# Kernel optimization log

Measured on AMD Instinct MI355X. Metric: run time of the kernel, lower is better.

## Reference

```python
import jax, jax.numpy as jnp
import numpy as np

N_A, N_B = 50000, 50000
E = 500000
IN, H, OUT, NGRAPHS = 128, 128, 10, 64
# (src_type, dst_type) per edge type, matching metadata[1]
EDGE_TYPES = [(0, 0), (0, 1), (1, 0), (1, 1)]
NUM_LAYERS = 2
NEG_SLOPE = 0.2  # GATConv leaky_relu slope


def setup_inputs() -> dict:
    key = jax.random.key(0)
    ks = jax.random.split(key, 16)
    ei = [jax.random.randint(ks[2 + e], (2, E), 0, 50000).astype(jnp.int32) for e in range(4)]
    return {
        "x_A": jax.random.normal(ks[0], (N_A, IN), jnp.float32),
        "x_B": jax.random.normal(ks[1], (N_B, IN), jnp.float32),
        "ei0": ei[0], "ei1": ei[1], "ei2": ei[2], "ei3": ei[3],
        "batch_A": jnp.sort(jax.random.randint(ks[6], (N_A,), 0, NGRAPHS)).astype(jnp.int32),
        "batch_B": jnp.sort(jax.random.randint(ks[7], (N_B,), 0, NGRAPHS)).astype(jnp.int32),
        "batch_size": NGRAPHS,
        "w_src": jax.random.normal(ks[8], (NUM_LAYERS, 4, IN, H), jnp.float32) * 0.05,
        "w_dst": jax.random.normal(ks[9], (NUM_LAYERS, 4, IN, H), jnp.float32) * 0.05,
        "att_src": jax.random.normal(ks[10], (NUM_LAYERS, 4, H), jnp.float32) * 0.05,
        "att_dst": jax.random.normal(ks[11], (NUM_LAYERS, 4, H), jnp.float32) * 0.05,
        "conv_bias": jax.random.normal(ks[12], (NUM_LAYERS, 4, H), jnp.float32) * 0.05,
        "wc": jax.random.normal(ks[13], (2 * H, OUT), jnp.float32) * 0.05,
        "bc": jax.random.normal(ks[14], (OUT,), jnp.float32) * 0.05,
    }


def gat_conv(x_src, x_dst, edge_index, ws, wd, a_s, a_d, b, num_dst):
    # PyG GATConv, heads=1, add_self_loops=False, aggr='mean'
    h_src = x_src @ ws            # [Ns, H]
    h_dst = x_dst @ wd            # [Nd, H]
    s_src = h_src @ a_s           # [Ns]
    s_dst = h_dst @ a_d           # [Nd]
    src, dst = edge_index[0], edge_index[1]
    score = jax.nn.leaky_relu(s_src[src] + s_dst[dst], NEG_SLOPE)  # [E]
    # segment softmax over destination nodes
    smax = jax.ops.segment_max(score, dst, num_segments=num_dst)
    ex = jnp.exp(score - smax[dst])
    denom = jax.ops.segment_sum(ex, dst, num_segments=num_dst)
    alpha = ex / denom[dst]
    msg = alpha[:, None] * h_src[src]                               # [E, H]
    summed = jax.ops.segment_sum(msg, dst, num_segments=num_dst)
    cnt = jax.ops.segment_sum(jnp.ones_like(alpha), dst, num_segments=num_dst)
    return summed / jnp.maximum(cnt, 1.0)[:, None] + b


def mean_pool(x, batch, batch_size):
    s = jax.ops.segment_sum(x, batch, num_segments=batch_size)
    c = jax.ops.segment_sum(jnp.ones((x.shape[0],), x.dtype), batch, num_segments=batch_size)
    return s / jnp.maximum(c, 1.0)[:, None]


def reference(x_A, x_B, ei0, ei1, ei2, ei3, batch_A, batch_B, batch_size,
              w_src, w_dst, att_src, att_dst, conv_bias, wc, bc):
    xs = [x_A, x_B]
    eis = [ei0, ei1, ei2, ei3]
    for L in range(NUM_LAYERS):
        outs = {0: [], 1: []}
        for e, (st, dt) in enumerate(EDGE_TYPES):
            o = gat_conv(xs[st], xs[dt], eis[e], w_src[L, e], w_dst[L, e],
                         att_src[L, e], att_dst[L, e], conv_bias[L, e], xs[dt].shape[0])
            outs[dt].append(o)
        # HeteroConv inter_aggr='mean' across edge types, then relu (dropout is identity in eval)
        xs = [jax.nn.relu(jnp.mean(jnp.stack(outs[t], 0), 0)) for t in (0, 1)]
    pooled = [mean_pool(xs[0], batch_A, batch_size), mean_pool(xs[1], batch_B, batch_size)]
    graph_emb = jnp.concatenate(pooled, axis=1)  # [B, 2H]
    return graph_emb @ wc + bc
```

## Files before the change

kernel.cpp:

```cpp
#include <hip/hip_runtime.h>
#include <hip/hip_bf16.h>

#define NN 50000
#define EE 500000
#define GG 64
#define NSL 50
#define SPAN 1000
#define NCH 125
#define EPG (EE / NCH)
#define NCNT (4 * NSL * NCH)
#define SCB ((NCNT + 255) / 256)

typedef __attribute__((ext_vector_type(8))) short bf16x8;
typedef __attribute__((ext_vector_type(4))) float f32x4;

__device__ __forceinline__ float wred_sum(float v) {
#pragma unroll
  for (int s = 32; s; s >>= 1) v += __shfl_xor(v, s, 64);
  return v;
}
__device__ __forceinline__ float gred_sum(float v) {
  v += __shfl_xor(v, 1, 64);
  v += __shfl_xor(v, 2, 64);
  v += __shfl_xor(v, 4, 64);
  v += __shfl_xor(v, 8, 64);
  return v;
}
__device__ __forceinline__ float gred_max(float v) {
  v = fmaxf(v, __shfl_xor(v, 1, 64));
  v = fmaxf(v, __shfl_xor(v, 2, 64));
  v = fmaxf(v, __shfl_xor(v, 4, 64));
  v = fmaxf(v, __shfl_xor(v, 8, 64));
  return v;
}

__device__ __forceinline__ short f2bf(float x) {
  __hip_bfloat16 b = __float2bfloat16(x);
  return *reinterpret_cast<short*>(&b);
}
__device__ __forceinline__ float bf2f(unsigned short s) {
  __hip_bfloat16 b = *reinterpret_cast<__hip_bfloat16*>(&s);
  return __bfloat162float(b);
}

__global__ __launch_bounds__(256) void v_kernel(const float* wdst, const float* adst, float* v) {
  int wv = (blockIdx.x * 256 + threadIdx.x) >> 6;
  int lane = threadIdx.x & 63;
  int le = wv >> 7, k = wv & 127;
  const float* W = wdst + (size_t)le * 16384 + k * 128;
  const float* a = adst + le * 128;
  float p = W[lane] * a[lane] + W[64 + lane] * a[64 + lane];
  p = wred_sum(p);
  if (lane == 0) v[le * 128 + k] = p;
}

__global__ __launch_bounds__(256) void wcvt_kernel(const float* wsrc, short* whiT, short* wloT) {
  int idx = blockIdx.x * 256 + threadIdx.x;
  int le = idx >> 14, rem = idx & 16383;
  int c = rem >> 7, k = rem & 127;
  float v = wsrc[(size_t)le * 16384 + k * 128 + c];
  short hi = f2bf(v);
  whiT[idx] = hi;
  wloT[idx] = f2bf(v - bf2f((unsigned short)hi));
}


__global__ __launch_bounds__(256) void pcount_kernel(const int* e0, const int* e1, const int* e2,
                                                     const int* e3, int* counts) {
  int t = blockIdx.y, ch = blockIdx.x;
  const int* ei = (t == 0 ? e0 : t == 1 ? e1 : t == 2 ? e2 : e3);
  const int* dst = ei + EE;
  __shared__ int cnt[NSL];
  for (int i = threadIdx.x; i < NSL; i += 256) cnt[i] = 0;
  __syncthreads();
  int i0 = ch * EPG;
  for (int i = i0 + threadIdx.x; i < i0 + EPG; i += 256) atomicAdd(&cnt[dst[i] / SPAN], 1);
  __syncthreads();
  for (int sl = threadIdx.x; sl < NSL; sl += 256) counts[(t * NSL + sl) * NCH + ch] = cnt[sl];
}

__global__ __launch_bounds__(256) void scan1_kernel(const int* counts, int* bsums) {
  int tid = threadIdx.x, lane = tid & 63, wid = tid >> 6;
  int idx = blockIdx.x * 256 + tid;
  int v = (idx < NCNT) ? counts[idx] : 0;
#pragma unroll
  for (int s = 32; s; s >>= 1) v += __shfl_xor(v, s, 64);
  __shared__ int ws[4];
  if (lane == 0) ws[wid] = v;
  __syncthreads();
  if (tid == 0) bsums[blockIdx.x] = ws[0] + ws[1] + ws[2] + ws[3];
}

__global__ void scan2_kernel(int* bsums) {
  __shared__ int s[SCB];
  int tid = threadIdx.x;
  if (tid < SCB) s[tid] = bsums[tid];
  __syncthreads();
  if (tid == 0) {
    int run = 0;
    for (int i = 0; i < SCB; i++) { int x = s[i]; s[i] = run; run += x; }
  }
  __syncthreads();
  if (tid < SCB) bsums[tid] = s[tid];
}

__global__ __launch_bounds__(256) void scan3_kernel(int* counts, const int* bsums, int* sliceptr) {
  int tid = threadIdx.x, lane = tid & 63, wid = tid >> 6;
  int idx = blockIdx.x * 256 + tid;
  int v = (idx < NCNT) ? counts[idx] : 0;
  int orig = v;
#pragma unroll
  for (int s = 1; s < 64; s <<= 1) { int u = __shfl_up(v, s, 64); if (lane >= s) v += u; }
  __shared__ int ws[4];
  if (lane == 63) ws[wid] = v;
  __syncthreads();
  int woff = (wid > 0 ? ws[0] : 0) + (wid > 1 ? ws[1] : 0) + (wid > 2 ? ws[2] : 0);
  int excl = bsums[blockIdx.x] + woff + v - orig;
  if (idx < NCNT) {
    counts[idx] = excl;
    if (idx % NCH == 0) {
      int g = idx / NCH;
      sliceptr[(g / NSL) * (NSL + 1) + (g % NSL)] = excl;
    }
  }
  if (blockIdx.x == 0 && tid < 4) sliceptr[tid * (NSL + 1) + NSL] = (tid + 1) * EE;
}

__global__ __launch_bounds__(256) void ppart_kernel(const int* e0, const int* e1, const int* e2,
                                                    const int* e3, const int* counts, int2* pairs) {
  int t = blockIdx.y, ch = blockIdx.x;
  const int* ei = (t == 0 ? e0 : t == 1 ? e1 : t == 2 ? e2 : e3);
  const int* srcr = ei;
  const int* dstr = ei + EE;
  __shared__ int cur[NSL];
  for (int i = threadIdx.x; i < NSL; i += 256) cur[i] = counts[(t * NSL + i) * NCH + ch];
  __syncthreads();
  int i0 = ch * EPG;
  for (int i = i0 + threadIdx.x; i < i0 + EPG; i += 256) {
    int d = dstr[i], s = srcr[i];
    int pos = atomicAdd(&cur[d / SPAN], 1);
    pairs[pos] = make_int2(s, d);
  }
}

__global__ __launch_bounds__(256) void pbuild_kernel(const int2* pairs, const int* sliceptr,
                                                     int* rowptr, int* col) {
  int t = blockIdx.y, sl = blockIdx.x;
  int n0 = sl * SPAN;
  int e0 = sliceptr[t * (NSL + 1) + sl], e1 = sliceptr[t * (NSL + 1) + sl + 1];
  int tid = threadIdx.x, lane = tid & 63, wid = tid >> 6;
  __shared__ int cnt[SPAN];
  __shared__ int wsum[4];
  for (int i = tid; i < SPAN; i += 256) cnt[i] = 0;
  __syncthreads();
  for (int e = e0 + tid; e < e1; e += 256) atomicAdd(&cnt[pairs[e].y - n0], 1);
  __syncthreads();
  int s0 = 0, s1 = 0, s2 = 0, s3 = 0, tot = 0;
  if (tid < SPAN / 4) {
    s0 = cnt[tid * 4]; s1 = cnt[tid * 4 + 1]; s2 = cnt[tid * 4 + 2]; s3 = cnt[tid * 4 + 3];
    tot = s0 + s1 + s2 + s3;
  }
  int v = tot;
#pragma unroll
  for (int sft = 1; sft < 64; sft <<= 1) { int u = __shfl_up(v, sft, 64); if (lane >= sft) v += u; }
  if (lane == 63) wsum[wid] = v;
  __syncthreads();
  int woffv = (wid > 0 ? wsum[0] : 0) + (wid > 1 ? wsum[1] : 0) + (wid > 2 ? wsum[2] : 0);
  int excl = v + woffv - tot;
  __syncthreads();
  if (tid < SPAN / 4) {
    cnt[tid * 4] = excl;
    cnt[tid * 4 + 1] = excl + s0;
    cnt[tid * 4 + 2] = excl + s0 + s1;
    cnt[tid * 4 + 3] = excl + s0 + s1 + s2;
  }
  __syncthreads();
  int base = e0 - t * EE;
  for (int n = tid; n < SPAN; n += 256) rowptr[(size_t)t * (NN + 1) + n0 + n] = base + cnt[n];
  if (sl == NSL - 1 && tid == 0) rowptr[(size_t)t * (NN + 1) + NN] = EE;
  __syncthreads();
  int* ct = col + (size_t)t * EE;
  for (int e = e0 + tid; e < e1; e += 256) {
    int2 p = pairs[e];
    int pos = base + atomicAdd(&cnt[p.y - n0], 1);
    ct[pos] = p.x;
  }
}

__global__ void gbound_kernel(const int* batchA, const int* batchB, int* gbA, int* gbB) {
  int t = threadIdx.x;
  if (t >= 130) return;
  int which = t / 65, g = t % 65;
  const int* b = which ? batchB : batchA;
  int* gb = which ? gbB : gbA;
  int lo = 0, hi = NN;
  while (lo < hi) { int mid = (lo + hi) >> 1; if (b[mid] < g) lo = mid + 1; else hi = mid; }
  gb[g] = lo;
}

#define SWZ(row, kb) ((((row) << 6) + (kb)) ^ (((row) & 7) << 4))
#define HSTRIDE 132

__device__ __forceinline__ void cvt8(const float4 a, const float4 b, bf16x8& hv, bf16x8& lv) {
  short h;
  h = f2bf(a.x); hv[0] = h; lv[0] = f2bf(a.x - bf2f((unsigned short)h));
  h = f2bf(a.y); hv[1] = h; lv[1] = f2bf(a.y - bf2f((unsigned short)h));
  h = f2bf(a.z); hv[2] = h; lv[2] = f2bf(a.z - bf2f((unsigned short)h));
  h = f2bf(a.w); hv[3] = h; lv[3] = f2bf(a.w - bf2f((unsigned short)h));
  h = f2bf(b.x); hv[4] = h; lv[4] = f2bf(b.x - bf2f((unsigned short)h));
  h = f2bf(b.y); hv[5] = h; lv[5] = f2bf(b.y - bf2f((unsigned short)h));
  h = f2bf(b.z); hv[6] = h; lv[6] = f2bf(b.z - bf2f((unsigned short)h));
  h = f2bf(b.w); hv[7] = h; lv[7] = f2bf(b.w - bf2f((unsigned short)h));
}

__global__ __launch_bounds__(256) void gemm_hs_kernel(
    const float* XA, const short* WhA, const short* WlA, const float* attA, unsigned short* hAo, float* sAo,
    const float* XB, const short* WhB, const short* WlB, const float* attB, unsigned short* hBo, float* sBo) {
  const float *X, *att;
  const short *Wh, *Wl;
  unsigned short* h;
  float* s_;
  if (blockIdx.z == 0) { X = XA; Wh = WhA; Wl = WlA; att = attA; h = hAo; s_ = sAo; }
  else                 { X = XB; Wh = WhB; Wl = WlB; att = attB; h = hBo; s_ = sBo; }

  __shared__ short smem[128 * HSTRIDE];
  short* Ah = smem;
  short* Al = smem + 4096;
  short* Bh = smem + 8192;
  short* Bl = smem + 12288;

  int tid = threadIdx.x;
  int l = tid & 63, w = tid >> 6;
  int arow = l & 15;
  int kb = (l >> 4) << 4;
  int row0 = blockIdx.x * 128;

  f32x4 acc[2][8];
#pragma unroll
  for (int i = 0; i < 2; i++)
#pragma unroll
    for (int j = 0; j < 8; j++) acc[i][j] = (f32x4){0.f, 0.f, 0.f, 0.f};

  float attr[8];
#pragma unroll
  for (int j = 0; j < 8; j++) attr[j] = att[j * 16 + arow];

  int sr = tid >> 1, half = tid & 1;
  int xrow = row0 + sr; xrow = xrow < NN ? xrow : NN - 1;
  const float* xbase = X + (size_t)xrow * 128 + half * 16;
  const short* whbase = Wh + sr * 128 + half * 16;
  const short* wlbase = Wl + sr * 128 + half * 16;
  int soff0 = SWZ(sr, half * 32);
  int soff1 = SWZ(sr, half * 32 + 16);

  for (int kt = 0; kt < 128; kt += 32) {
    __syncthreads();
    float4 f0 = *(const float4*)(xbase + kt);
    float4 f1 = *(const float4*)(xbase + kt + 4);
    float4 f2 = *(const float4*)(xbase + kt + 8);
    float4 f3 = *(const float4*)(xbase + kt + 12);
    bf16x8 hv0, lv0, hv1, lv1;
    cvt8(f0, f1, hv0, lv0);
    cvt8(f2, f3, hv1, lv1);
    *(bf16x8*)((char*)Ah + soff0) = hv0;
    *(bf16x8*)((char*)Ah + soff1) = hv1;
    *(bf16x8*)((char*)Al + soff0) = lv0;
    *(bf16x8*)((char*)Al + soff1) = lv1;
    *(bf16x8*)((char*)Bh + soff0) = *(const bf16x8*)(whbase + kt);
    *(bf16x8*)((char*)Bh + soff1) = *(const bf16x8*)(whbase + kt + 8);
    *(bf16x8*)((char*)Bl + soff0) = *(const bf16x8*)(wlbase + kt);
    *(bf16x8*)((char*)Bl + soff1) = *(const bf16x8*)(wlbase + kt + 8);
    __syncthreads();

    bf16x8 ah[2], al[2];
#pragma unroll
    for (int i = 0; i < 2; i++) {
      int row = w * 32 + i * 16 + arow;
      ah[i] = *(bf16x8*)((char*)Ah + SWZ(row, kb));
      al[i] = *(bf16x8*)((char*)Al + SWZ(row, kb));
    }
#pragma unroll
    for (int j = 0; j < 8; j++) {
      int colr = j * 16 + arow;
      bf16x8 bh = *(bf16x8*)((char*)Bh + SWZ(colr, kb));
      bf16x8 bl = *(bf16x8*)((char*)Bl + SWZ(colr, kb));
#pragma unroll
      for (int i = 0; i < 2; i++) {
        acc[i][j] = __builtin_amdgcn_mfma_f32_16x16x32_bf16(ah[i], bh, acc[i][j], 0, 0, 0);
        acc[i][j] = __builtin_amdgcn_mfma_f32_16x16x32_bf16(ah[i], bl, acc[i][j], 0, 0, 0);
        acc[i][j] = __builtin_amdgcn_mfma_f32_16x16x32_bf16(al[i], bh, acc[i][j], 0, 0, 0);
      }
    }
  }

  __syncthreads();
#pragma unroll
  for (int i = 0; i < 2; i++) {
#pragma unroll
    for (int r = 0; r < 4; r++) {
      int lrow = w * 32 + i * 16 + ((l >> 4) << 2) + r;
      int row = row0 + lrow;
      float p = 0.f;
#pragma unroll
      for (int j = 0; j < 8; j++) p += acc[i][j][r] * attr[j];
      p += __shfl_xor(p, 1, 64);
      p += __shfl_xor(p, 2, 64);
      p += __shfl_xor(p, 4, 64);
      p += __shfl_xor(p, 8, 64);
      if (row < NN && arow == 0) s_[row] = p;
#pragma unroll
      for (int j = 0; j < 8; j++) smem[lrow * HSTRIDE + j * 16 + arow] = f2bf(acc[i][j][r]);
    }
  }
  __syncthreads();
#pragma unroll
  for (int it = 0; it < 8; it++) {
    int idx = it * 256 + tid;
    int lrow = idx >> 4, c8 = idx & 15;
    int row = row0 + lrow;
    if (row < NN)
      *(bf16x8*)(h + (size_t)row * 128 + c8 * 8) = *(const bf16x8*)(smem + lrow * HSTRIDE + c8 * 8);
  }
}

#define ACC8(a, uv, wv)                             \
  do {                                              \
    a[0] += wv * __uint_as_float(uv.x << 16);       \
    a[1] += wv * __uint_as_float(uv.x & 0xffff0000u); \
    a[2] += wv * __uint_as_float(uv.y << 16);       \
    a[3] += wv * __uint_as_float(uv.y & 0xffff0000u); \
    a[4] += wv * __uint_as_float(uv.z << 16);       \
    a[5] += wv * __uint_as_float(uv.z & 0xffff0000u); \
    a[6] += wv * __uint_as_float(uv.w << 16);       \
    a[7] += wv * __uint_as_float(uv.w & 0xffff0000u); \
  } while (0)

__global__ __launch_bounds__(256) void agg_kernel(
    const float* xdst,
    const int* rpA, const int* colA, const unsigned short* hA_, const float* sA_, const float* vA, const float* bA,
    const int* rpB, const int* colB, const unsigned short* hB_, const float* sB_, const float* vB, const float* bB,
    float* Y) {
  int lane = threadIdx.x & 63;
  int q = lane & 15;
  int gb = lane & 48;
  int node = blockIdx.x * 16 + (threadIdx.x >> 4);
  if (node >= NN) return;
  int d0 = q * 8;
  const float* xr = xdst + (size_t)node * 128 + d0;
  float4 xv0 = *(const float4*)(xr);
  float4 xv1 = *(const float4*)(xr + 4);
  float outv[8] = {0.f, 0.f, 0.f, 0.f, 0.f, 0.f, 0.f, 0.f};

  for (int t = 0; t < 2; t++) {
    const int* rp = t ? rpB : rpA;
    const int* cl = t ? colB : colA;
    const unsigned short* h = t ? hB_ : hA_;
    const float* ss = t ? sB_ : sA_;
    const float* v = t ? vB : vA;
    const uint4* hq = (const uint4*)h + q;

    float4 v0 = *(const float4*)(v + d0);
    float4 v1 = *(const float4*)(v + d0 + 4);
    float part = xv0.x * v0.x + xv0.y * v0.y + xv0.z * v0.z + xv0.w * v0.w +
                 xv1.x * v1.x + xv1.y * v1.y + xv1.z * v1.z + xv1.w * v1.w;
    float sd = gred_sum(part);

    int start = rp[node], end = rp[node + 1];
    int deg = end - start;

    int src0 = 0, src1 = 0;
    float s0v = 0.f, s1v = 0.f;
    float m = -3.4e38f;
    {
      int i = start + q;
      if (i < end) { src0 = cl[i]; float s = ss[src0] + sd; s = s >= 0.f ? s : 0.2f * s; s0v = s; m = fmaxf(m, s); }
      i += 16;
      if (i < end) { src1 = cl[i]; float s = ss[src1] + sd; s = s >= 0.f ? s : 0.2f * s; s1v = s; m = fmaxf(m, s); }
      for (i = start + 32 + q; i < end; i += 16) {
        float s = ss[cl[i]] + sd; s = s >= 0.f ? s : 0.2f * s; m = fmaxf(m, s);
      }
    }
    m = gred_max(m);

    float ex0 = (start + q < end) ? __expf(s0v - m) : 0.f;
    float ex1 = (start + 16 + q < end) ? __expf(s1v - m) : 0.f;
    float dsum = ex0 + ex1;
    float a[8] = {0.f, 0.f, 0.f, 0.f, 0.f, 0.f, 0.f, 0.f};

    int c0 = min(16, deg);
    for (int j = 0; j < c0; j++) {
      int sj = __shfl(src0, gb + j, 64);
      float exj = __shfl(ex0, gb + j, 64);
      uint4 uv = hq[(size_t)sj * 16];
      ACC8(a, uv, exj);
    }
    int c1 = min(16, deg - 16);
    for (int j = 0; j < c1; j++) {
      int sj = __shfl(src1, gb + j, 64);
      float exj = __shfl(ex1, gb + j, 64);
      uint4 uv = hq[(size_t)sj * 16];
      ACC8(a, uv, exj);
    }
    for (int base2 = start + 32; base2 < end; base2 += 16) {
      int i2 = base2 + q;
      int srcT = 0;
      float exT = 0.f;
      if (i2 < end) {
        srcT = cl[i2];
        float s = ss[srcT] + sd; s = s >= 0.f ? s : 0.2f * s;
        exT = __expf(s - m);
      }
      dsum += exT;
      int cT = min(16, end - base2);
      for (int j = 0; j < cT; j++) {
        int sj = __shfl(srcT, gb + j, 64);
        float exj = __shfl(exT, gb + j, 64);
        uint4 uv = hq[(size_t)sj * 16];
        ACC8(a, uv, exj);
      }
    }

    float denom = gred_sum(dsum);
    float inv = (deg > 0) ? 0.5f / (denom * (float)deg) : 0.f;
    const float* b = t ? bB : bA;
#pragma unroll
    for (int k2 = 0; k2 < 8; k2++) outv[k2] += a[k2] * inv + 0.5f * b[d0 + k2];
  }

  float4 o0 = make_float4(fmaxf(outv[0], 0.f), fmaxf(outv[1], 0.f), fmaxf(outv[2], 0.f), fmaxf(outv[3], 0.f));
  float4 o1 = make_float4(fmaxf(outv[4], 0.f), fmaxf(outv[5], 0.f), fmaxf(outv[6], 0.f), fmaxf(outv[7], 0.f));
  *(float4*)(Y + (size_t)node * 128 + d0) = o0;
  *(float4*)(Y + (size_t)node * 128 + d0 + 4) = o1;
}

__global__ __launch_bounds__(128) void pool_part_kernel(const float* XA_, const float* XB_,
                                                        const int* gbA, const int* gbB,
                                                        float* pooled) {
  int t = blockIdx.y, g = blockIdx.x, c = blockIdx.z;
  const float* X = t ? XB_ : XA_;
  const int* gb = t ? gbB : gbA;
  int n0 = gb[g], n1 = gb[g + 1];
  int dim = threadIdx.x;
  float s = 0.f;
  for (int node = n0 + c; node < n1; node += 8) s += X[(size_t)node * 128 + dim];
  atomicAdd(&pooled[g * 256 + t * 128 + dim], s);
}

__global__ void final_kernel(const float* pooled, const int* gbA, const int* gbB,
                             const float* wc, const float* bc, float* out) {
  int tid = blockIdx.x * blockDim.x + threadIdx.x;
  if (tid >= GG * 10) return;
  int g = tid / 10, o = tid % 10;
  float invA = 1.f / fmaxf((float)(gbA[g + 1] - gbA[g]), 1.f);
  float invB = 1.f / fmaxf((float)(gbB[g + 1] - gbB[g]), 1.f);
  float acc = bc[o];
  for (int k = 0; k < 256; k++)
    acc += pooled[g * 256 + k] * (k < 128 ? invA : invB) * wc[k * 10 + o];
  out[g * 10 + o] = acc;
}

extern "C" void kernel_launch(void* const* d_in, const int* in_sizes, int n_in,
                              void* d_out, int out_size, void* d_ws, size_t ws_size,
                              hipStream_t stream) {
  const float* xA = (const float*)d_in[0];
  const float* xB = (const float*)d_in[1];
  const int* ei0 = (const int*)d_in[2];
  const int* ei1 = (const int*)d_in[3];
  const int* ei2 = (const int*)d_in[4];
  const int* ei3 = (const int*)d_in[5];
  const int* batchA = (const int*)d_in[6];
  const int* batchB = (const int*)d_in[7];
  const float* wsrc = (const float*)d_in[9];
  const float* wdst = (const float*)d_in[10];
  const float* attsrc = (const float*)d_in[11];
  const float* attdst = (const float*)d_in[12];
  const float* cbias = (const float*)d_in[13];
  const float* wc = (const float*)d_in[14];
  const float* bc = (const float*)d_in[15];
  float* out = (float*)d_out;

  char* ws = (char*)d_ws;
  size_t off = 0;
  auto alloc = [&](size_t bytes) { size_t o = off; off += (bytes + 255) & ~(size_t)255; return o; };
  size_t o_rowptr = alloc((size_t)4 * (NN + 1) * 4);
  size_t o_col    = alloc((size_t)4 * EE * 4);
  size_t o_cnts   = alloc((size_t)NCNT * 4);
  size_t o_bsums  = alloc((size_t)SCB * 4);
  size_t o_slptr  = alloc((size_t)4 * (NSL + 1) * 4);
  size_t o_v      = alloc((size_t)8 * 128 * 4);
  size_t o_whiT   = alloc((size_t)8 * 16384 * 2);
  size_t o_wloT   = alloc((size_t)8 * 16384 * 2);
  size_t o_hA     = alloc((size_t)NN * 128 * 2);
  size_t o_hB     = alloc((size_t)NN * 128 * 2);
  size_t o_sA     = alloc((size_t)NN * 4);
  size_t o_sB     = alloc((size_t)NN * 4);
  size_t o_Xa1    = alloc((size_t)NN * 128 * 4);
  size_t o_Xb1    = alloc((size_t)NN * 128 * 4);
  size_t o_Xa2    = alloc((size_t)NN * 128 * 4);
  size_t o_Xb2    = alloc((size_t)NN * 128 * 4);
  size_t o_pooled = alloc((size_t)GG * 256 * 4);
  size_t o_gb     = alloc((size_t)2 * (GG + 1) * 4);

  int* rowptr = (int*)(ws + o_rowptr);
  int* col = (int*)(ws + o_col);
  int* counts = (int*)(ws + o_cnts);
  int* bsums = (int*)(ws + o_bsums);
  int* sliceptr = (int*)(ws + o_slptr);
  float* vv = (float*)(ws + o_v);
  short* whiT = (short*)(ws + o_whiT);
  short* wloT = (short*)(ws + o_wloT);
  unsigned short* hA = (unsigned short*)(ws + o_hA);
  unsigned short* hB = (unsigned short*)(ws + o_hB);
  int2* pairs = (int2*)(ws + o_hA);
  float* sA = (float*)(ws + o_sA);
  float* sB = (float*)(ws + o_sB);
  float* Xa1 = (float*)(ws + o_Xa1);
  float* Xb1 = (float*)(ws + o_Xb1);
  float* Xa2 = (float*)(ws + o_Xa2);
  float* Xb2 = (float*)(ws + o_Xb2);
  float* pooled = (float*)(ws + o_pooled);
  int* gbA = (int*)(ws + o_gb);
  int* gbB = gbA + (GG + 1);

  hipMemsetAsync(pooled, 0, (size_t)GG * 256 * 4, stream);

  v_kernel<<<256, 256, 0, stream>>>(wdst, attdst, vv);
  wcvt_kernel<<<512, 256, 0, stream>>>(wsrc, whiT, wloT);
  gbound_kernel<<<1, 192, 0, stream>>>(batchA, batchB, gbA, gbB);
  pcount_kernel<<<dim3(NCH, 4), 256, 0, stream>>>(ei0, ei1, ei2, ei3, counts);
  scan1_kernel<<<SCB, 256, 0, stream>>>(counts, bsums);
  scan2_kernel<<<1, 128, 0, stream>>>(bsums);
  scan3_kernel<<<SCB, 256, 0, stream>>>(counts, bsums, sliceptr);
  ppart_kernel<<<dim3(NCH, 4), 256, 0, stream>>>(ei0, ei1, ei2, ei3, counts, pairs);
  pbuild_kernel<<<dim3(NSL, 4), 256, 0, stream>>>(pairs, sliceptr, rowptr, col);

  int gemm_gx = (NN + 127) / 128;
  int agg_gx = (NN + 15) / 16;

  for (int L = 0; L < 2; L++) {
    const float* X0 = (L == 0) ? xA : Xa1;
    const float* X1 = (L == 0) ? xB : Xb1;
    float* Y0 = (L == 0) ? Xa1 : Xa2;
    float* Y1 = (L == 0) ? Xb1 : Xb2;

    gemm_hs_kernel<<<dim3(gemm_gx, 1, 2), 256, 0, stream>>>(
        X0, whiT + (size_t)(L * 4 + 0) * 16384, wloT + (size_t)(L * 4 + 0) * 16384,
        attsrc + (L * 4 + 0) * 128, hA, sA,
        X1, whiT + (size_t)(L * 4 + 2) * 16384, wloT + (size_t)(L * 4 + 2) * 16384,
        attsrc + (L * 4 + 2) * 128, hB, sB);
    agg_kernel<<<agg_gx, 256, 0, stream>>>(
        X0,
        rowptr + (size_t)0 * (NN + 1), col + (size_t)0 * EE, hA, sA, vv + (L * 4 + 0) * 128, cbias + (L * 4 + 0) * 128,
        rowptr + (size_t)2 * (NN + 1), col + (size_t)2 * EE, hB, sB, vv + (L * 4 + 2) * 128, cbias + (L * 4 + 2) * 128,
        Y0);

    gemm_hs_kernel<<<dim3(gemm_gx, 1, 2), 256, 0, stream>>>(
        X0, whiT + (size_t)(L * 4 + 1) * 16384, wloT + (size_t)(L * 4 + 1) * 16384,
        attsrc + (L * 4 + 1) * 128, hA, sA,
        X1, whiT + (size_t)(L * 4 + 3) * 16384, wloT + (size_t)(L * 4 + 3) * 16384,
        attsrc + (L * 4 + 3) * 128, hB, sB);
    agg_kernel<<<agg_gx, 256, 0, stream>>>(
        X1,
        rowptr + (size_t)1 * (NN + 1), col + (size_t)1 * EE, hA, sA, vv + (L * 4 + 1) * 128, cbias + (L * 4 + 1) * 128,
        rowptr + (size_t)3 * (NN + 1), col + (size_t)3 * EE, hB, sB, vv + (L * 4 + 3) * 128, cbias + (L * 4 + 3) * 128,
        Y1);
  }

  pool_part_kernel<<<dim3(GG, 2, 8), 128, 0, stream>>>(Xa2, Xb2, gbA, gbB, pooled);
  final_kernel<<<3, 256, 0, stream>>>(pooled, gbA, gbB, wc, bc, out);
}
```

Baseline: 395.4 us.

## Merge per-layer GEMMs into one launch and drop softmax max pass

Each layer's four source-projection GEMMs now run as one 4-slice launch writing into separate h/s buffers, replacing two launches that reused shared buffers. The aggregation kernel drops the segment-max pass and computes exp(score) directly in a single pass, with the gather loop unrolled by four so more row loads are in flight. This removes a launch and a second read of col/score per node, but skipping max subtraction risks overflow if scores grow large, and the h buffer footprint doubles.

New measurement: 390.4 us. About the same (-1.3%).

```diff
diff --git a/kernel.cpp b/kernel.cpp
--- a/kernel.cpp
+++ b/kernel.cpp
@@ -24,13 +24,6 @@
   v += __shfl_xor(v, 2, 64);
   v += __shfl_xor(v, 4, 64);
   v += __shfl_xor(v, 8, 64);
-  return v;
-}
-__device__ __forceinline__ float gred_max(float v) {
-  v = fmaxf(v, __shfl_xor(v, 1, 64));
-  v = fmaxf(v, __shfl_xor(v, 2, 64));
-  v = fmaxf(v, __shfl_xor(v, 4, 64));
-  v = fmaxf(v, __shfl_xor(v, 8, 64));
   return v;
 }
 
@@ -214,14 +207,17 @@
 }
 
 __global__ __launch_bounds__(256) void gemm_hs_kernel(
-    const float* XA, const short* WhA, const short* WlA, const float* attA, unsigned short* hAo, float* sAo,
-    const float* XB, const short* WhB, const short* WlB, const float* attB, unsigned short* hBo, float* sBo) {
-  const float *X, *att;
-  const short *Wh, *Wl;
-  unsigned short* h;
-  float* s_;
-  if (blockIdx.z == 0) { X = XA; Wh = WhA; Wl = WlA; att = attA; h = hAo; s_ = sAo; }
-  else                 { X = XB; Wh = WhB; Wl = WlB; att = attB; h = hBo; s_ = sBo; }
+    const float* X0_, const float* X1_,
+    const short* whiT, const short* wloT,
+    const float* attsrc,
+    unsigned short* h4, float* s4) {
+  int e = blockIdx.z;
+  const float* X = (e < 2) ? X0_ : X1_;
+  const short* Wh = whiT + (size_t)e * 16384;
+  const short* Wl = wloT + (size_t)e * 16384;
+  const float* att = attsrc + e * 128;
+  unsigned short* h = h4 + (size_t)e * NN * 128;
+  float* s_ = s4 + (size_t)e * NN;
 
   __shared__ short smem[128 * HSTRIDE];
   short* Ah = smem;
@@ -368,55 +364,41 @@
     int start = rp[node], end = rp[node + 1];
     int deg = end - start;
 
-    int src0 = 0, src1 = 0;
-    float s0v = 0.f, s1v = 0.f;
-    float m = -3.4e38f;
-    {
-      int i = start + q;
-      if (i < end) { src0 = cl[i]; float s = ss[src0] + sd; s = s >= 0.f ? s : 0.2f * s; s0v = s; m = fmaxf(m, s); }
-      i += 16;
-      if (i < end) { src1 = cl[i]; float s = ss[src1] + sd; s = s >= 0.f ? s : 0.2f * s; s1v = s; m = fmaxf(m, s); }
-      for (i = start + 32 + q; i < end; i += 16) {
-        float s = ss[cl[i]] + sd; s = s >= 0.f ? s : 0.2f * s; m = fmaxf(m, s);
+    float dsum = 0.f;
+    float a[8] = {0.f, 0.f, 0.f, 0.f, 0.f, 0.f, 0.f, 0.f};
+
+    for (int base2 = start; base2 < end; base2 += 16) {
+      int i = base2 + q;
+      int src = 0;
+      float ex = 0.f;
+      if (i < end) {
+        src = cl[i];
+        float s = ss[src] + sd;
+        s = (s >= 0.f) ? s : 0.2f * s;
+        ex = __expf(s);
       }
-    }
-    m = gred_max(m);
-
-    float ex0 = (start + q < end) ? __expf(s0v - m) : 0.f;
-    float ex1 = (start + 16 + q < end) ? __expf(s1v - m) : 0.f;
-    float dsum = ex0 + ex1;
-    float a[8] = {0.f, 0.f, 0.f, 0.f, 0.f, 0.f, 0.f, 0.f};
-
-    int c0 = min(16, deg);
-    for (int j = 0; j < c0; j++) {
-      int sj = __shfl(src0, gb + j, 64);
-      float exj = __shfl(ex0, gb + j, 64);
-      uint4 uv = hq[(size_t)sj * 16];
-      ACC8(a, uv, exj);
-    }
-    int c1 = min(16, deg - 16);
-    for (int j = 0; j < c1; j++) {
-      int sj = __shfl(src1, gb + j, 64);
-      float exj = __shfl(ex1, gb + j, 64);
-      uint4 uv = hq[(size_t)sj * 16];
-      ACC8(a, uv, exj);
-    }
-    for (int base2 = start + 32; base2 < end; base2 += 16) {
-      int i2 = base2 + q;
-      int srcT = 0;
-      float exT = 0.f;
-      if (i2 < end) {
-        srcT = cl[i2];
-        float s = ss[srcT] + sd; s = s >= 0.f ? s : 0.2f * s;
-        exT = __expf(s - m);
+      dsum += ex;
+      int cT = min(16, end - base2);
+      int j = 0;
+      for (; j + 3 < cT; j += 4) {
+        int sj0 = __shfl(src, gb + j, 64);     float e0 = __shfl(ex, gb + j, 64);
+        int sj1 = __shfl(src, gb + j + 1, 64); float e1 = __shfl(ex, gb + j + 1, 64);
+        int sj2 = __shfl(src, gb + j + 2, 64); float e2 = __shfl(ex, gb + j + 2, 64);
+        int sj3 = __shfl(src, gb + j + 3, 64); float e3 = __shfl(ex, gb + j + 3, 64);
+        uint4 uv0 = hq[(size_t)sj0 * 16];
+        uint4 uv1 = hq[(size_t)sj1 * 16];
+        uint4 uv2 = hq[(size_t)sj2 * 16];
+        uint4 uv3 = hq[(size_t)sj3 * 16];
+        ACC8(a, uv0, e0);
+        ACC8(a, uv1, e1);
+        ACC8(a, uv2, e2);
+        ACC8(a, uv3, e3);
       }
-      dsum += exT;
-      int cT = min(16, end - base2);
-      for (int j = 0; j < cT; j++) {
-        int sj = __shfl(srcT, gb + j, 64);
-        float exj = __shfl(exT, gb + j, 64);
+      for (; j < cT; j++) {
+        int sj = __shfl(src, gb + j, 64);
+        float ej = __shfl(ex, gb + j, 64);
         uint4 uv = hq[(size_t)sj * 16];
-        ACC8(a, uv, exj);
+        ACC8(a, uv, ej);
       }
     }
 
@@ -490,10 +472,8 @@
   size_t o_v      = alloc((size_t)8 * 128 * 4);
   size_t o_whiT   = alloc((size_t)8 * 16384 * 2);
   size_t o_wloT   = alloc((size_t)8 * 16384 * 2);
-  size_t o_hA     = alloc((size_t)NN * 128 * 2);
-  size_t o_hB     = alloc((size_t)NN * 128 * 2);
-  size_t o_sA     = alloc((size_t)NN * 4);
-  size_t o_sB     = alloc((size_t)NN * 4);
+  size_t o_h4     = alloc((size_t)4 * NN * 128 * 2);
+  size_t o_s4     = alloc((size_t)4 * NN * 4);
   size_t o_Xa1    = alloc((size_t)NN * 128 * 4);
   size_t o_Xb1    = alloc((size_t)NN * 128 * 4);
   size_t o_Xa2    = alloc((size_t)NN * 128 * 4);
@@ -509,11 +489,9 @@
   float* vv = (float*)(ws + o_v);
   short* whiT = (short*)(ws + o_whiT);
   short* wloT = (short*)(ws + o_wloT);
-  unsigned short* hA = (unsigned short*)(ws + o_hA);
-  unsigned short* hB = (unsigned short*)(ws + o_hB);
-  int2* pairs = (int2*)(ws + o_hA);
-  float* sA = (float*)(ws + o_sA);
-  float* sB = (float*)(ws + o_sB);
+  unsigned short* h4 = (unsigned short*)(ws + o_h4);
+  float* s4 = (float*)(ws + o_s4);
+  int2* pairs = (int2*)(ws + o_h4);
   float* Xa1 = (float*)(ws + o_Xa1);
   float* Xb1 = (float*)(ws + o_Xb1);
   float* Xa2 = (float*)(ws + o_Xa2);
@@ -543,26 +521,24 @@
     float* Y0 = (L == 0) ? Xa1 : Xa2;
     float* Y1 = (L == 0) ? Xb1 : Xb2;
 
-    gemm_hs_kernel<<<dim3(gemm_gx, 1, 2), 256, 0, stream>>>(
-        X0, whiT + (size_t)(L * 4 + 0) * 16384, wloT + (size_t)(L * 4 + 0) * 16384,
-        attsrc + (L * 4 + 0) * 128, hA, sA,
-        X1, whiT + (size_t)(L * 4 + 2) * 16384, wloT + (size_t)(L * 4 + 2) * 16384,
-        attsrc + (L * 4 + 2) * 128, hB, sB);
+    gemm_hs_kernel<<<dim3(gemm_gx, 1, 4), 256, 0, stream>>>(
+        X0, X1, whiT + (size_t)L * 4 * 16384, wloT + (size_t)L * 4 * 16384,
+        attsrc + L * 4 * 128, h4, s4);
+
     agg_kernel<<<agg_gx, 256, 0, stream>>>(
         X0,
-        rowptr + (size_t)0 * (NN + 1), col + (size_t)0 * EE, hA, sA, vv + (L * 4 + 0) * 128, cbias + (L * 4 + 0) * 128,
-        rowptr + (size_t)2 * (NN + 1), col + (size_t)2 * EE, hB, sB, vv + (L * 4 + 2) * 128, cbias + (L * 4 + 2) * 128,
+        rowptr + (size_t)0 * (NN + 1), col + (size_t)0 * EE, h4 + (size_t)0 * NN * 128, s4 + (size_t)0 * NN,
+        vv + (L * 4 + 0) * 128, cbias + (L * 4 + 0) * 128,
+        rowptr + (size_t)2 * (NN + 1), col + (size_t)2 * EE, h4 + (size_t)2 * NN * 128, s4 + (size_t)2 * NN,
+        vv + (L * 4 + 2) * 128, cbias + (L * 4 + 2) * 128,
         Y0);
 
-    gemm_hs_kernel<<<dim3(gemm_gx, 1, 2), 256, 0, stream>>>(
-        X0, whiT + (size_t)(L * 4 + 1) * 16384, wloT + (size_t)(L * 4 + 1) * 16384,
-        attsrc + (L * 4 + 1) * 128, hA, sA,
-        X1, whiT + (size_t)(L * 4 + 3) * 16384, wloT + (size_t)(L * 4 + 3) * 16384,
-        attsrc + (L * 4 + 3) * 128, hB, sB);
     agg_kernel<<<agg_gx, 256, 0, stream>>>(
         X1,
-        rowptr + (size_t)1 * (NN + 1), col + (size_t)1 * EE, hA, sA, vv + (L * 4 + 1) * 128, cbias + (L * 4 + 1) * 128,
-        rowptr + (size_t)3 * (NN + 1), col + (size_t)3 * EE, hB, sB, vv + (L * 4 + 3) * 128, cbias + (L * 4 + 3) * 128,
+        rowptr + (size_t)1 * (NN + 1), col + (size_t)1 * EE, h4 + (size_t)1 * NN * 128, s4 + (size_t)1 * NN,
+        vv + (L * 4 + 1) * 128, cbias + (L * 4 + 1) * 128,
+        rowptr + (size_t)3 * (NN + 1), col + (size_t)3 * EE, h4 + (size_t)3 * NN * 128, s4 + (size_t)3 * NN,
+        vv + (L * 4 + 3) * 128, cbias + (L * 4 + 3) * 128,
         Y1);
   }
 
```
